# Kernel optimization log

Measured on AMD Instinct MI355X. Metric: run time of the kernel, lower is better.

Reference implementation:

```python
import jax, jax.numpy as jnp
import numpy as np

B, L, H, E = 4, 1024, 8, 64


def setup_inputs() -> dict:
    key = jax.random.key(0)
    kq, kk, kv = jax.random.split(key, 3)
    queries = jax.random.normal(kq, (B, L, H, E), dtype=jnp.float32)
    keys = jax.random.normal(kk, (B, L, H, E), dtype=jnp.float32)
    values = jax.random.normal(kv, (B, L, H, E), dtype=jnp.float32)
    attn_mask = jnp.zeros((1,), dtype=bool)  # unused by the module
    return {"queries": queries, "keys": keys, "values": values, "attn_mask": attn_mask}


def _spectral_interaction(queries, keys, values):
    # queries/keys/values: [B, L, H, E] (L == S here, so the torch truncation is a no-op)
    b, l, h, e = queries.shape
    qh = jnp.transpose(queries, (0, 2, 1, 3))  # [B,H,L,E]
    kh = jnp.transpose(keys[:, :l], (0, 2, 1, 3))  # [B,H,L,E]
    # cosine-similarity score matrix, exponentiated: exp(q.k / (|q||k|))
    q_norm = jnp.linalg.norm(qh, axis=-1, keepdims=True)  # [B,H,L,1]
    k_norm = jnp.linalg.norm(kh, axis=-1, keepdims=True)  # [B,H,L,1]
    dot_num = jnp.einsum('bhle,bhse->bhls', qh, kh)        # [B,H,L,L]
    dot_den = q_norm * jnp.swapaxes(k_norm, -1, -2)        # [B,H,L,L] via broadcast
    sim = jnp.exp(dot_num / dot_den)                       # [B,H,L,L]

    # FFT-domain double softmax over frequency bins
    inter_fft = jnp.fft.rfft(sim, axis=-1).real            # [B,H,L,F], F=L//2+1
    scale = 1.0 / np.sqrt(e)
    A = jax.nn.softmax(
        jnp.sum(jax.nn.softmax(scale * inter_fft, axis=-1), axis=-2),
        axis=-1,
    )                                                      # [B,H,F]  (dropout = identity in eval)
    A = A[:, :, None, :]                                   # [B,H,1,F]

    # gate the real part of the value spectrum, keep imag part, reconstruct
    vh = jnp.transpose(values[:, :l], (0, 2, 3, 1))        # [B,H,E,L]
    v_fft = jnp.fft.rfft(vh, axis=-1)                      # [B,H,E,F] complex
    Vc = jax.lax.complex(A * v_fft.real, v_fft.imag)       # [B,H,E,F]
    V = jnp.fft.irfft(Vc, n=l, axis=-1)                    # [B,H,E,L]
    return jnp.transpose(V, (0, 3, 2, 1))                  # [B,L,E,H] (matches torch permute(0,3,2,1))


def reference(queries, keys, values, attn_mask):
    # attn_mask is unused by the original forward
    return _spectral_interaction(queries, keys, values)
```

## Files before the change

### kernel.cpp

```cpp
#include <hip/hip_runtime.h>
#include <hip/hip_bf16.h>
#include <math.h>

#define B_ 4
#define L_ 1024
#define H_ 8
#define E_ 64
#define N_ 1024
#define NF_ 513
#define SCALE_ 0.125f
#define HE_ (H_ * E_)
#define ZP_ 1104

typedef _Float16 f16x8 __attribute__((ext_vector_type(8)));
typedef float f32x4 __attribute__((ext_vector_type(4)));

__device__ __forceinline__ int dr4(int x) {
    const int r = (int)(__brev((unsigned)x) >> 22);
    return ((r & 0x155) << 1) | ((r >> 1) & 0x155);
}

__device__ __forceinline__ int PD(int i) { return i + (i >> 4) + (i >> 6); }

__device__ __forceinline__ float2 cmulw(float2 v, float2 w, float dir) {
    const float wi = dir * w.y;
    return make_float2(v.x * w.x - v.y * wi, v.x * wi + v.y * w.x);
}

__device__ __forceinline__ void r4c(const float2 x0, const float2 x1,
                                    const float2 x2, const float2 x3,
                                    const float dir,
                                    float2& y0, float2& y1, float2& y2, float2& y3) {
    const float ax = x0.x + x2.x, ay = x0.y + x2.y;
    const float bx = x0.x - x2.x, by = x0.y - x2.y;
    const float cx = x1.x + x3.x, cy = x1.y + x3.y;
    const float dx = x1.x - x3.x, dy = x1.y - x3.y;
    y0 = make_float2(ax + cx, ay + cy);
    y2 = make_float2(ax - cx, ay - cy);
    y1 = make_float2(bx - dir * dy, by + dir * dx);
    y3 = make_float2(bx + dir * dy, by - dir * dx);
}

__device__ __forceinline__ void fill_tw(float2* tw, int t) {
    for (int i = t; i < 1024; i += 256) {
        float sv, cv;
        sincosf(6.283185307179586f * (float)i / 1024.0f, &sv, &cv);
        tw[PD(i)] = make_float2(cv, sv);
    }
}

__device__ __forceinline__ void wfft_dit4(float2* z, const float2* tw, int lane, float dir) {
    #pragma unroll
    for (int st = 0; st < 5; ++st) {
        const int l2q = 2 * st, qs = 1 << l2q;
        const int step = 1 << (8 - l2q);
        #pragma unroll
        for (int ib = 0; ib < 4; ++ib) {
            const int j = lane + 64 * ib;
            const int pos = j & (qs - 1);
            const int base = ((j >> l2q) << (l2q + 2)) + pos;
            const int i0 = PD(base), i1 = PD(base + qs), i2 = PD(base + 2 * qs), i3 = PD(base + 3 * qs);
            float2 x0 = z[i0], x1 = z[i1], x2 = z[i2], x3 = z[i3];
            if (st) {
                x1 = cmulw(x1, tw[PD(pos * step)], dir);
                x2 = cmulw(x2, tw[PD(2 * pos * step)], dir);
                x3 = cmulw(x3, tw[PD(3 * pos * step)], dir);
            }
            float2 y0, y1, y2, y3;
            r4c(x0, x1, x2, x3, dir, y0, y1, y2, y3);
            z[i0] = y0; z[i1] = y1; z[i2] = y2; z[i3] = y3;
        }
        __builtin_amdgcn_wave_barrier();
    }
}

__device__ __forceinline__ void wfft_dif4(float2* z, const float2* tw, int lane, float dir) {
    #pragma unroll
    for (int st = 4; st >= 0; --st) {
        const int l2q = 2 * st, qs = 1 << l2q;
        const int step = 1 << (8 - l2q);
        #pragma unroll
        for (int ib = 0; ib < 4; ++ib) {
            const int j = lane + 64 * ib;
            const int pos = j & (qs - 1);
            const int base = ((j >> l2q) << (l2q + 2)) + pos;
            const int i0 = PD(base), i1 = PD(base + qs), i2 = PD(base + 2 * qs), i3 = PD(base + 3 * qs);
            const float2 x0 = z[i0], x1 = z[i1], x2 = z[i2], x3 = z[i3];
            float2 s0, s1, s2, s3;
            r4c(x0, x1, x2, x3, dir, s0, s1, s2, s3);
            if (st) {
                s1 = cmulw(s1, tw[PD(pos * step)], dir);
                s2 = cmulw(s2, tw[PD(2 * pos * step)], dir);
                s3 = cmulw(s3, tw[PD(3 * pos * step)], dir);
            }
            z[i0] = s0; z[i1] = s1; z[i2] = s2; z[i3] = s3;
        }
        __builtin_amdgcn_wave_barrier();
    }
}

__global__ __launch_bounds__(256) void k_prep(const float* __restrict__ K,
                                              _Float16* __restrict__ Kh) {
    const int i = blockIdx.x * 256 + threadIdx.x;
    if (i >= B_ * L_ * H_) return;
    const float* p = K + (size_t)i * E_;
    float ss = 0.0f;
    #pragma unroll
    for (int j = 0; j < 16; ++j) {
        const float4 v = *(const float4*)(p + j * 4);
        ss += v.x * v.x + v.y * v.y + v.z * v.z + v.w * v.w;
    }
    const float r = rsqrtf(ss);
    _Float16* out = Kh + (size_t)i * E_;
    #pragma unroll
    for (int e = 0; e < E_; e += 8) {
        const float4 x = *(const float4*)(p + e);
        const float4 y = *(const float4*)(p + e + 4);
        f16x8 o;
        o[0] = (_Float16)(x.x * r); o[1] = (_Float16)(x.y * r);
        o[2] = (_Float16)(x.z * r); o[3] = (_Float16)(x.w * r);
        o[4] = (_Float16)(y.x * r); o[5] = (_Float16)(y.y * r);
        o[6] = (_Float16)(y.z * r); o[7] = (_Float16)(y.w * r);
        *(f16x8*)(out + e) = o;
    }
}

__global__ __attribute__((amdgpu_flat_work_group_size(256, 256), amdgpu_waves_per_eu(2, 3)))
void k_qkfft(const float* __restrict__ Q,
             const _Float16* __restrict__ Kh,
             float* __restrict__ G) {
    __shared__ float2 s_z[4 * ZP_];
    __shared__ float2 s_tw[ZP_];
    __shared__ float s_acc[NF_];

    const int t = threadIdx.x;
    const int bid = blockIdx.x;
    const int bh = bid >> 6;
    const int chunk = bid & 63;
    const int b = bh >> 3, h = bh & 7;
    const int l0 = chunk * 16;

    const int c = t & 15;
    const int g = (t >> 4) & 3;
    const int w = t >> 6;
    const int lane = t & 63;

    fill_tw(s_tw, t);
    for (int kk = t; kk < NF_; kk += 256) s_acc[kk] = 0.0f;

    const float* qrow = Q + (((size_t)b * L_ + l0 + c) * H_ + h) * E_;
    const float4 x0 = *(const float4*)(qrow + g * 8);
    const float4 y0 = *(const float4*)(qrow + g * 8 + 4);
    const float4 x1 = *(const float4*)(qrow + 32 + g * 8);
    const float4 y1 = *(const float4*)(qrow + 32 + g * 8 + 4);
    float ss = x0.x * x0.x + x0.y * x0.y + x0.z * x0.z + x0.w * x0.w
             + y0.x * y0.x + y0.y * y0.y + y0.z * y0.z + y0.w * y0.w
             + x1.x * x1.x + x1.y * x1.y + x1.z * x1.z + x1.w * x1.w
             + y1.x * y1.x + y1.y * y1.y + y1.z * y1.z + y1.w * y1.w;
    ss += __shfl_xor(ss, 16);
    ss += __shfl_xor(ss, 32);
    const float qn = rsqrtf(ss);
    f16x8 af0, af1;
    af0[0] = (_Float16)(x0.x * qn); af0[1] = (_Float16)(x0.y * qn);
    af0[2] = (_Float16)(x0.z * qn); af0[3] = (_Float16)(x0.w * qn);
    af0[4] = (_Float16)(y0.x * qn); af0[5] = (_Float16)(y0.y * qn);
    af0[6] = (_Float16)(y0.z * qn); af0[7] = (_Float16)(y0.w * qn);
    af1[0] = (_Float16)(x1.x * qn); af1[1] = (_Float16)(x1.y * qn);
    af1[2] = (_Float16)(x1.z * qn); af1[3] = (_Float16)(x1.w * qn);
    af1[4] = (_Float16)(y1.x * qn); af1[5] = (_Float16)(y1.y * qn);
    af1[6] = (_Float16)(y1.z * qn); af1[7] = (_Float16)(y1.w * qn);

    f32x4 acc[16];
    #pragma unroll
    for (int n = 0; n < 16; ++n) acc[n] = (f32x4){0.0f, 0.0f, 0.0f, 0.0f};

    #pragma unroll
    for (int n = 0; n < 16; ++n) {
        const int j = w * 256 + n * 16 + c;
        const int s = dr4(j);
        const f16x8* bp = (const f16x8*)(Kh + (((size_t)b * L_ + s) * H_ + h) * E_);
        const f16x8 b0 = bp[g];
        const f16x8 b1 = bp[4 + g];
        acc[n] = __builtin_amdgcn_mfma_f32_16x16x32_f16(af0, b0, acc[n], 0, 0, 0);
        acc[n] = __builtin_amdgcn_mfma_f32_16x16x32_f16(af1, b1, acc[n], 0, 0, 0);
        if ((n & 3) == 3) __builtin_amdgcn_sched_barrier(0);
    }

    #pragma unroll
    for (int n = 0; n < 16; ++n) {
        #pragma unroll
        for (int r = 0; r < 4; ++r) acc[n][r] = __expf(acc[n][r]);
    }

    float gacc[8];
    #pragma unroll
    for (int ib = 0; ib < 8; ++ib) gacc[ib] = 0.0f;
    float gN = 0.0f;

    float2* zw = s_z + w * ZP_;
    const float dir = -1.0f;

    #pragma unroll
    for (int rr = 0; rr < 2; ++rr) {
        __syncthreads();
        {
            const int gq = g - 2 * rr;
            if (gq == 0 || gq == 1) {
                float2* z01 = s_z + (2 * gq) * ZP_;
                #pragma unroll
                for (int n = 0; n < 16; ++n) {
                    const int ps = PD(w * 256 + n * 16 + c);
                    z01[ps]       = make_float2(acc[n][0], acc[n][1]);
                    z01[ZP_ + ps] = make_float2(acc[n][2], acc[n][3]);
                }
            }
        }
        __syncthreads();

        wfft_dit4(zw, s_tw, lane, dir);

        const float mA = SCALE_ * zw[0].x;
        const float mB = SCALE_ * zw[0].y;
        float pA[8], pB[8], sA = 0.0f, sB = 0.0f;
        #pragma unroll
        for (int ib = 0; ib < 8; ++ib) {
            const int k = lane + 64 * ib;
            const int kp = (N_ - k) & (N_ - 1);
            const float2 X1 = zw[PD(k)];
            const float2 X2 = zw[PD(kp)];
            pA[ib] = __expf(SCALE_ * 0.5f * (X1.x + X2.x) - mA);
            pB[ib] = __expf(SCALE_ * 0.5f * (X1.y + X2.y) - mB);
            sA += pA[ib]; sB += pB[ib];
        }
        float pAN = 0.0f, pBN = 0.0f;
        if (lane == 0) {
            const float2 XN = zw[PD(512)];
            pAN = __expf(SCALE_ * XN.x - mA);
            pBN = __expf(SCALE_ * XN.y - mB);
            sA += pAN; sB += pBN;
        }
        #pragma unroll
        for (int off = 32; off > 0; off >>= 1) {
            sA += __shfl_xor(sA, off);
            sB += __shfl_xor(sB, off);
        }
        const float iA = 1.0f / sA, iB = 1.0f / sB;
        #pragma unroll
        for (int ib = 0; ib < 8; ++ib) gacc[ib] += pA[ib] * iA + pB[ib] * iB;
        if (lane == 0) gN += pAN * iA + pBN * iB;
    }

    #pragma unroll
    for (int ib = 0; ib < 8; ++ib) atomicAdd(&s_acc[lane + 64 * ib], gacc[ib]);
    if (lane == 0) atomicAdd(&s_acc[512], gN);
    __syncthreads();

    float* Gp = G + (size_t)bh * NF_;
    for (int kk = t; kk < NF_; kk += 256) atomicAdd(&Gp[kk], s_acc[kk]);
}

__global__ __launch_bounds__(256) void k_vfft(const float* __restrict__ V,
                                              const float* __restrict__ G,
                                              float* __restrict__ Out) {
    __shared__ float2 s_zv[4 * ZP_];
    __shared__ float2 s_tw[ZP_];
    __shared__ float s_A[NF_];
    __shared__ float s_red[8];

    const int t = threadIdx.x;
    const int bid = blockIdx.x;
    const int bh = bid >> 3, pg = bid & 7;
    const int b = bh >> 3, h = bh & 7;
    const int w = t >> 6, lane = t & 63;
    const int e0 = 2 * (pg * 4 + w);

    fill_tw(s_tw, t);

    {
        const float* Gp = G + (size_t)bh * NF_;
        const float g0 = Gp[t];
        const float g1 = Gp[t + 256];
        const float g2 = (t == 0) ? Gp[512] : -1e30f;
        float m = fmaxf(fmaxf(g0, g1), g2);
        #pragma unroll
        for (int off = 32; off > 0; off >>= 1) m = fmaxf(m, __shfl_xor(m, off));
        if (lane == 0) s_red[w] = m;
        __syncthreads();
        m = fmaxf(fmaxf(s_red[0], s_red[1]), fmaxf(s_red[2], s_red[3]));
        const float p0 = __expf(g0 - m), p1 = __expf(g1 - m);
        const float p2 = (t == 0) ? __expf(g2 - m) : 0.0f;
        float s = p0 + p1 + p2;
        #pragma unroll
        for (int off = 32; off > 0; off >>= 1) s += __shfl_xor(s, off);
        __syncthreads();
        if (lane == 0) s_red[4 + w] = s;
        __syncthreads();
        s = s_red[4] + s_red[5] + s_red[6] + s_red[7];
        const float inv = 1.0f / s;
        s_A[t] = p0 * inv;
        s_A[t + 256] = p1 * inv;
        if (t == 0) s_A[512] = p2 * inv;
    }
    __syncthreads();

    float2* z = s_zv + w * ZP_;

    #pragma unroll
    for (int jb = 0; jb < 16; ++jb) {
        const int s = lane + 64 * jb;
        const float* vp = V + (((size_t)b * L_ + s) * H_ + h) * E_ + e0;
        z[PD(dr4(s))] = make_float2(vp[0], vp[1]);
    }
    __builtin_amdgcn_wave_barrier();

    wfft_dit4(z, s_tw, lane, -1.0f);

    #pragma unroll
    for (int ib = 0; ib < 8; ++ib) {
        const int k = lane + 64 * ib;
        const int kp = (N_ - k) & (N_ - 1);
        const int ik = PD(k), ikp = PD(kp);
        const float2 X1 = z[ik];
        const float2 X2 = z[ikp];
        const float reV1 = 0.5f * (X1.x + X2.x);
        const float imV1 = 0.5f * (X1.y - X2.y);
        const float reV2 = 0.5f * (X1.y + X2.y);
        const float imV2 = 0.5f * (X2.x - X1.x);
        const float a = s_A[k];
        z[ik] = make_float2(a * reV1 - imV2, imV1 + a * reV2);
        if (kp != k)
            z[ikp] = make_float2(a * reV1 + imV2, -imV1 + a * reV2);
    }
    if (lane == 0) {
        const float2 X = z[PD(512)];
        const float a = s_A[512];
        z[PD(512)] = make_float2(a * X.x, a * X.y);
    }
    __builtin_amdgcn_wave_barrier();

    wfft_dif4(z, s_tw, lane, +1.0f);

    const float invN = 1.0f / (float)N_;
    #pragma unroll
    for (int jb = 0; jb < 16; ++jb) {
        const int p = lane + 64 * jb;
        const int l = dr4(p);
        const float2 r = z[PD(p)];
        const size_t o = (((size_t)b * L_ + l) * E_ + e0) * H_ + h;
        Out[o] = r.x * invN;
        Out[o + H_] = r.y * invN;
    }
}

extern "C" void kernel_launch(void* const* d_in, const int* in_sizes, int n_in,
                              void* d_out, int out_size, void* d_ws, size_t ws_size,
                              hipStream_t stream) {
    const float* Q = (const float*)d_in[0];
    const float* K = (const float*)d_in[1];
    const float* V = (const float*)d_in[2];
    float* out = (float*)d_out;

    float* ws = (float*)d_ws;
    float* G     = ws;
    _Float16* Kh = (_Float16*)(ws + B_ * H_ * NF_);

    hipMemsetAsync(G, 0, (size_t)B_ * H_ * NF_ * sizeof(float), stream);
    k_prep<<<(B_ * L_ * H_ + 255) / 256, 256, 0, stream>>>(K, Kh);
    k_qkfft<<<B_ * H_ * (L_ / 16), 256, 0, stream>>>(Q, Kh, G);
    k_vfft<<<B_ * H_ * (E_ / 8), 256, 0, stream>>>(V, G, out);
}
```

Baseline: 136.4 us.

## Halve FFT shared buffer and run block-cooperative FFT over four rounds

The QK-FFT kernel stops having each of its four waves run its own 1024-point FFT on a private shared buffer. Instead the whole 256-thread block cooperates on two packed FFTs per round, with a barrier between radix-4 stages, over four serial rounds, and softmax sums are reduced across waves through a small shared array. This halves the s_z shared allocation and raises the waves-per-EU hint, aiming for more resident blocks per CU. The cost is many more __syncthreads per block and four serialized rounds instead of two.

```diff
diff --git a/kernel.cpp b/kernel.cpp
--- a/kernel.cpp
+++ b/kernel.cpp
@@ -125,13 +125,14 @@
     }
 }
 
-__global__ __attribute__((amdgpu_flat_work_group_size(256, 256), amdgpu_waves_per_eu(2, 3)))
+__global__ __attribute__((amdgpu_flat_work_group_size(256, 256), amdgpu_waves_per_eu(2, 5)))
 void k_qkfft(const float* __restrict__ Q,
              const _Float16* __restrict__ Kh,
              float* __restrict__ G) {
-    __shared__ float2 s_z[4 * ZP_];
+    __shared__ float2 s_z[2 * ZP_];
     __shared__ float2 s_tw[ZP_];
     __shared__ float s_acc[NF_];
+    __shared__ float s_red[16];
 
     const int t = threadIdx.x;
     const int bid = blockIdx.x;
@@ -143,7 +144,7 @@
     const int c = t & 15;
     const int g = (t >> 4) & 3;
     const int w = t >> 6;
-    const int lane = t & 63;
+    const int lane = t & 63, wid = w;
 
     fill_tw(s_tw, t);
     for (int kk = t; kk < NF_; kk += 256) s_acc[kk] = 0.0f;
@@ -192,67 +193,88 @@
         for (int r = 0; r < 4; ++r) acc[n][r] = __expf(acc[n][r]);
     }
 
-    float gacc[8];
-    #pragma unroll
-    for (int ib = 0; ib < 8; ++ib) gacc[ib] = 0.0f;
-    float gN = 0.0f;
-
-    float2* zw = s_z + w * ZP_;
     const float dir = -1.0f;
 
-    #pragma unroll
-    for (int rr = 0; rr < 2; ++rr) {
-        __syncthreads();
-        {
-            const int gq = g - 2 * rr;
-            if (gq == 0 || gq == 1) {
-                float2* z01 = s_z + (2 * gq) * ZP_;
-                #pragma unroll
-                for (int n = 0; n < 16; ++n) {
-                    const int ps = PD(w * 256 + n * 16 + c);
-                    z01[ps]       = make_float2(acc[n][0], acc[n][1]);
-                    z01[ZP_ + ps] = make_float2(acc[n][2], acc[n][3]);
-                }
-            }
-        }
-        __syncthreads();
-
-        wfft_dit4(zw, s_tw, lane, dir);
-
-        const float mA = SCALE_ * zw[0].x;
-        const float mB = SCALE_ * zw[0].y;
-        float pA[8], pB[8], sA = 0.0f, sB = 0.0f;
-        #pragma unroll
-        for (int ib = 0; ib < 8; ++ib) {
-            const int k = lane + 64 * ib;
-            const int kp = (N_ - k) & (N_ - 1);
-            const float2 X1 = zw[PD(k)];
-            const float2 X2 = zw[PD(kp)];
-            pA[ib] = __expf(SCALE_ * 0.5f * (X1.x + X2.x) - mA);
-            pB[ib] = __expf(SCALE_ * 0.5f * (X1.y + X2.y) - mB);
-            sA += pA[ib]; sB += pB[ib];
-        }
-        float pAN = 0.0f, pBN = 0.0f;
+    #pragma unroll 1
+    for (int rr = 0; rr < 4; ++rr) {
+        __syncthreads();
+        if (g == rr) {
+            #pragma unroll
+            for (int n = 0; n < 16; ++n) {
+                const int ps = PD(w * 256 + n * 16 + c);
+                s_z[ps]       = make_float2(acc[n][0], acc[n][1]);
+                s_z[ZP_ + ps] = make_float2(acc[n][2], acc[n][3]);
+            }
+        }
+        __syncthreads();
+
+        #pragma unroll
+        for (int st = 0; st < 5; ++st) {
+            const int l2q = 2 * st, qs = 1 << l2q;
+            const int pos = t & (qs - 1);
+            const int base = ((t >> l2q) << (l2q + 2)) + pos;
+            const int i0 = PD(base), i1 = PD(base + qs), i2 = PD(base + 2 * qs), i3 = PD(base + 3 * qs);
+            float2 w1, w2, w3;
+            if (st) {
+                const int step = 1 << (8 - l2q);
+                w1 = s_tw[PD(pos * step)];
+                w2 = s_tw[PD(2 * pos * step)];
+                w3 = s_tw[PD(3 * pos * step)];
+            }
+            #pragma unroll
+            for (int q = 0; q < 2; ++q) {
+                float2* z = s_z + q * ZP_;
+                float2 a0 = z[i0], a1 = z[i1], a2 = z[i2], a3 = z[i3];
+                if (st) { a1 = cmulw(a1, w1, dir); a2 = cmulw(a2, w2, dir); a3 = cmulw(a3, w3, dir); }
+                float2 b0, b1, b2, b3;
+                r4c(a0, a1, a2, a3, dir, b0, b1, b2, b3);
+                z[i0] = b0; z[i1] = b1; z[i2] = b2; z[i3] = b3;
+            }
+            __syncthreads();
+        }
+
+        const int iT = PD(t), iTn = PD((N_ - t) & (N_ - 1));
+        const int iU = PD(t + 256), iUn = PD(768 - t);
+        float p[4][2], pm[4], sm[4];
+        #pragma unroll
+        for (int q = 0; q < 2; ++q) {
+            const float2* z = s_z + q * ZP_;
+            const float2 X0 = z[iT], X0n = z[iTn], X1 = z[iU], X1n = z[iUn];
+            const float2 DC = z[0];
+            const float2 XN = z[PD(512)];
+            const float mA = SCALE_ * DC.x, mB = SCALE_ * DC.y;
+            p[2 * q][0]     = __expf(SCALE_ * 0.5f * (X0.x + X0n.x) - mA);
+            p[2 * q][1]     = __expf(SCALE_ * 0.5f * (X1.x + X1n.x) - mA);
+            p[2 * q + 1][0] = __expf(SCALE_ * 0.5f * (X0.y + X0n.y) - mB);
+            p[2 * q + 1][1] = __expf(SCALE_ * 0.5f * (X1.y + X1n.y) - mB);
+            pm[2 * q]     = __expf(SCALE_ * XN.x - mA);
+            pm[2 * q + 1] = __expf(SCALE_ * XN.y - mB);
+            sm[2 * q]     = p[2 * q][0] + p[2 * q][1] + ((t == 0) ? pm[2 * q] : 0.0f);
+            sm[2 * q + 1] = p[2 * q + 1][0] + p[2 * q + 1][1] + ((t == 0) ? pm[2 * q + 1] : 0.0f);
+        }
+        #pragma unroll
+        for (int off = 32; off > 0; off >>= 1) {
+            #pragma unroll
+            for (int q2 = 0; q2 < 4; ++q2) sm[q2] += __shfl_xor(sm[q2], off);
+        }
         if (lane == 0) {
-            const float2 XN = zw[PD(512)];
-            pAN = __expf(SCALE_ * XN.x - mA);
-            pBN = __expf(SCALE_ * XN.y - mB);
-            sA += pAN; sB += pBN;
-        }
-        #pragma unroll
-        for (int off = 32; off > 0; off >>= 1) {
-            sA += __shfl_xor(sA, off);
-            sB += __shfl_xor(sB, off);
-        }
-        const float iA = 1.0f / sA, iB = 1.0f / sB;
-        #pragma unroll
-        for (int ib = 0; ib < 8; ++ib) gacc[ib] += pA[ib] * iA + pB[ib] * iB;
-        if (lane == 0) gN += pAN * iA + pBN * iB;
-    }
-
-    #pragma unroll
-    for (int ib = 0; ib < 8; ++ib) atomicAdd(&s_acc[lane + 64 * ib], gacc[ib]);
-    if (lane == 0) atomicAdd(&s_acc[512], gN);
+            #pragma unroll
+            for (int q2 = 0; q2 < 4; ++q2) s_red[4 * q2 + wid] = sm[q2];
+        }
+        __syncthreads();
+        float add0 = 0.0f, add1 = 0.0f, addm = 0.0f;
+        #pragma unroll
+        for (int q2 = 0; q2 < 4; ++q2) {
+            const float inv = 1.0f / (s_red[4 * q2] + s_red[4 * q2 + 1] +
+                                      s_red[4 * q2 + 2] + s_red[4 * q2 + 3]);
+            add0 += p[q2][0] * inv;
+            add1 += p[q2][1] * inv;
+            addm += pm[q2] * inv;
+        }
+        s_acc[t]       += add0;
+        s_acc[t + 256] += add1;
+        if (t == 0) s_acc[512] += addm;
+    }
     __syncthreads();
 
     float* Gp = G + (size_t)bh * NF_;
```

After: 123.7 us. 1.1x faster.

## Replace per-row FFT of similarity rows with cosine-DFT matmul on MFMA

Applied to the files above, without the earlier changes.

The real part of the rFFT of each similarity row is now computed as a matmul against a precomputed fp16 cosine table on MFMA units, replacing the shared-memory radix-4 FFT. The similarity tile is staged in LDS as fp16, and the softmax max shift uses the DC bin, which is the row sum. Block size doubles to 32 query rows, and the per-bin reductions now go straight to global atomics. This adds a cosine-table kernel, reduces precision through fp16 cosines and fp16 exp values, and does roughly 4x more arithmetic than the FFT, relying on matrix-core throughput to cover it.

```diff
diff --git a/kernel.cpp b/kernel.cpp
--- a/kernel.cpp
+++ b/kernel.cpp
@@ -1,5 +1,6 @@
 #include <hip/hip_runtime.h>
 #include <hip/hip_bf16.h>
+#include <hip/hip_fp16.h>
 #include <math.h>
 
 #define B_ 4
@@ -11,22 +12,22 @@
 #define SCALE_ 0.125f
 #define HE_ (H_ * E_)
 #define ZP_ 1104
+#define NBPAD_ 576
+#define SIMP_ 1032
 
 typedef _Float16 f16x8 __attribute__((ext_vector_type(8)));
+typedef _Float16 f16x4 __attribute__((ext_vector_type(4)));
 typedef float f32x4 __attribute__((ext_vector_type(4)));
 
 __device__ __forceinline__ int dr4(int x) {
     const int r = (int)(__brev((unsigned)x) >> 22);
     return ((r & 0x155) << 1) | ((r >> 1) & 0x155);
 }
-
 __device__ __forceinline__ int PD(int i) { return i + (i >> 4) + (i >> 6); }
-
 __device__ __forceinline__ float2 cmulw(float2 v, float2 w, float dir) {
     const float wi = dir * w.y;
     return make_float2(v.x * w.x - v.y * wi, v.x * wi + v.y * w.x);
 }
-
 __device__ __forceinline__ void r4c(const float2 x0, const float2 x1,
                                     const float2 x2, const float2 x3,
                                     const float dir,
@@ -40,7 +41,6 @@
     y1 = make_float2(bx - dir * dy, by + dir * dx);
     y3 = make_float2(bx + dir * dy, by - dir * dx);
 }
-
 __device__ __forceinline__ void fill_tw(float2* tw, int t) {
     for (int i = t; i < 1024; i += 256) {
         float sv, cv;
@@ -48,7 +48,6 @@
         tw[PD(i)] = make_float2(cv, sv);
     }
 }
-
 __device__ __forceinline__ void wfft_dit4(float2* z, const float2* tw, int lane, float dir) {
     #pragma unroll
     for (int st = 0; st < 5; ++st) {
@@ -56,7 +55,8 @@
         const int step = 1 << (8 - l2q);
         #pragma unroll
         for (int ib = 0; ib < 4; ++ib) {
-            const int j = lane + 64 * ib;
+            const int j = (st == 0) ? (((lane & 15) << 2) | (lane >> 4)) + 64 * ib
+                                    : lane + 64 * ib;
             const int pos = j & (qs - 1);
             const int base = ((j >> l2q) << (l2q + 2)) + pos;
             const int i0 = PD(base), i1 = PD(base + qs), i2 = PD(base + 2 * qs), i3 = PD(base + 3 * qs);
@@ -73,7 +73,6 @@
         __builtin_amdgcn_wave_barrier();
     }
 }
-
 __device__ __forceinline__ void wfft_dif4(float2* z, const float2* tw, int lane, float dir) {
     #pragma unroll
     for (int st = 4; st >= 0; --st) {
@@ -81,7 +80,8 @@
         const int step = 1 << (8 - l2q);
         #pragma unroll
         for (int ib = 0; ib < 4; ++ib) {
-            const int j = lane + 64 * ib;
+            const int j = (st == 0) ? (((lane & 15) << 2) | (lane >> 4)) + 64 * ib
+                                    : lane + 64 * ib;
             const int pos = j & (qs - 1);
             const int base = ((j >> l2q) << (l2q + 2)) + pos;
             const int i0 = PD(base), i1 = PD(base + qs), i2 = PD(base + 2 * qs), i3 = PD(base + 3 * qs);
@@ -99,6 +99,23 @@
     }
 }
 
+__global__ __launch_bounds__(256) void k_ccos(_Float16* __restrict__ Cc) {
+    const int bin = blockIdx.x;
+    const int t = threadIdx.x;
+    f16x4 o;
+    if (bin > 512) {
+        o[0] = o[1] = o[2] = o[3] = (_Float16)0.0f;
+    } else {
+        #pragma unroll
+        for (int j = 0; j < 4; ++j) {
+            const int s = 4 * t + j;
+            const int m = (bin * s) & 1023;
+            o[j] = (_Float16)cosf((float)m * 0.006135923151542565f);
+        }
+    }
+    *(f16x4*)(Cc + (size_t)bin * 1024 + 4 * t) = o;
+}
+
 __global__ __launch_bounds__(256) void k_prep(const float* __restrict__ K,
                                               _Float16* __restrict__ Kh) {
     const int i = blockIdx.x * 256 + threadIdx.x;
@@ -125,138 +142,175 @@
     }
 }
 
-__global__ __attribute__((amdgpu_flat_work_group_size(256, 256), amdgpu_waves_per_eu(2, 3)))
+template<int NU>
+__device__ __forceinline__ void qk_group(const _Float16* __restrict__ Cc,
+                                         const _Float16* __restrict__ s_sim,
+                                         int ntb, int c, int g,
+                                         float F0a, float F0b,
+                                         float& rs0, float& rs1,
+                                         __half2 (&e)[NU * 4]) {
+    f32x4 acc[2][NU];
+    #pragma unroll
+    for (int u = 0; u < NU; ++u) {
+        acc[0][u] = (f32x4){0.f, 0.f, 0.f, 0.f};
+        acc[1][u] = (f32x4){0.f, 0.f, 0.f, 0.f};
+    }
+    #pragma unroll 4
+    for (int kt = 0; kt < 32; ++kt) {
+        const int ko = kt * 32 + g * 8;
+        const f16x8 B0 = *(const f16x8*)(s_sim + (size_t)c * SIMP_ + ko);
+        const f16x8 B1 = *(const f16x8*)(s_sim + (size_t)(16 + c) * SIMP_ + ko);
+        #pragma unroll
+        for (int u = 0; u < NU; ++u) {
+            const f16x8 A = *(const f16x8*)(Cc + (size_t)((ntb + u) * 16 + c) * 1024 + ko);
+            acc[0][u] = __builtin_amdgcn_mfma_f32_16x16x32_f16(A, B0, acc[0][u], 0, 0, 0);
+            acc[1][u] = __builtin_amdgcn_mfma_f32_16x16x32_f16(A, B1, acc[1][u], 0, 0, 0);
+        }
+    }
+    #pragma unroll
+    for (int u = 0; u < NU; ++u) {
+        #pragma unroll
+        for (int r = 0; r < 4; ++r) {
+            const int bin = (ntb + u) * 16 + 4 * g + r;
+            const float e0 = __expf(SCALE_ * (acc[0][u][r] - F0a));
+            const float e1 = __expf(SCALE_ * (acc[1][u][r] - F0b));
+            if (bin <= 512) { rs0 += e0; rs1 += e1; }
+            e[u * 4 + r] = __floats2half2_rn(e0, e1);
+        }
+    }
+}
+
+template<int NU>
+__device__ __forceinline__ void qk_accum(float* __restrict__ Gp,
+                                         const __half2 (&e)[NU * 4],
+                                         int ntb, int c, int g,
+                                         float inva, float invb) {
+    #pragma unroll
+    for (int u = 0; u < NU; ++u) {
+        #pragma unroll
+        for (int r = 0; r < 4; ++r) {
+            const int bin = (ntb + u) * 16 + 4 * g + r;
+            const float2 ef = __half22float2(e[u * 4 + r]);
+            float v = ef.x * inva + ef.y * invb;
+            v += __shfl_xor(v, 1);
+            v += __shfl_xor(v, 2);
+            v += __shfl_xor(v, 4);
+            v += __shfl_xor(v, 8);
+            if (c == 0 && bin <= 512) atomicAdd(&Gp[bin], v);
+        }
+    }
+}
+
+__global__ __attribute__((amdgpu_flat_work_group_size(256, 256), amdgpu_waves_per_eu(2, 2)))
 void k_qkfft(const float* __restrict__ Q,
              const _Float16* __restrict__ Kh,
+             const _Float16* __restrict__ Cc,
              float* __restrict__ G) {
-    __shared__ float2 s_z[4 * ZP_];
-    __shared__ float2 s_tw[ZP_];
-    __shared__ float s_acc[NF_];
+    __shared__ _Float16 s_sim[32 * SIMP_];
+    __shared__ float s_F0p[4][32];
+    __shared__ float s_F0[32];
+    __shared__ float s_rs[4][32];
+    __shared__ float s_inv[32];
 
     const int t = threadIdx.x;
     const int bid = blockIdx.x;
-    const int bh = bid >> 6;
-    const int chunk = bid & 63;
+    const int bh = bid >> 5;
+    const int l0 = (bid & 31) * 32;
     const int b = bh >> 3, h = bh & 7;
-    const int l0 = chunk * 16;
-
     const int c = t & 15;
     const int g = (t >> 4) & 3;
     const int w = t >> 6;
-    const int lane = t & 63;
-
-    fill_tw(s_tw, t);
-    for (int kk = t; kk < NF_; kk += 256) s_acc[kk] = 0.0f;
-
-    const float* qrow = Q + (((size_t)b * L_ + l0 + c) * H_ + h) * E_;
-    const float4 x0 = *(const float4*)(qrow + g * 8);
-    const float4 y0 = *(const float4*)(qrow + g * 8 + 4);
-    const float4 x1 = *(const float4*)(qrow + 32 + g * 8);
-    const float4 y1 = *(const float4*)(qrow + 32 + g * 8 + 4);
-    float ss = x0.x * x0.x + x0.y * x0.y + x0.z * x0.z + x0.w * x0.w
-             + y0.x * y0.x + y0.y * y0.y + y0.z * y0.z + y0.w * y0.w
-             + x1.x * x1.x + x1.y * x1.y + x1.z * x1.z + x1.w * x1.w
-             + y1.x * y1.x + y1.y * y1.y + y1.z * y1.z + y1.w * y1.w;
-    ss += __shfl_xor(ss, 16);
-    ss += __shfl_xor(ss, 32);
-    const float qn = rsqrtf(ss);
-    f16x8 af0, af1;
-    af0[0] = (_Float16)(x0.x * qn); af0[1] = (_Float16)(x0.y * qn);
-    af0[2] = (_Float16)(x0.z * qn); af0[3] = (_Float16)(x0.w * qn);
-    af0[4] = (_Float16)(y0.x * qn); af0[5] = (_Float16)(y0.y * qn);
-    af0[6] = (_Float16)(y0.z * qn); af0[7] = (_Float16)(y0.w * qn);
-    af1[0] = (_Float16)(x1.x * qn); af1[1] = (_Float16)(x1.y * qn);
-    af1[2] = (_Float16)(x1.z * qn); af1[3] = (_Float16)(x1.w * qn);
-    af1[4] = (_Float16)(y1.x * qn); af1[5] = (_Float16)(y1.y * qn);
-    af1[6] = (_Float16)(y1.z * qn); af1[7] = (_Float16)(y1.w * qn);
-
-    f32x4 acc[16];
-    #pragma unroll
-    for (int n = 0; n < 16; ++n) acc[n] = (f32x4){0.0f, 0.0f, 0.0f, 0.0f};
-
-    #pragma unroll
-    for (int n = 0; n < 16; ++n) {
-        const int j = w * 256 + n * 16 + c;
-        const int s = dr4(j);
-        const f16x8* bp = (const f16x8*)(Kh + (((size_t)b * L_ + s) * H_ + h) * E_);
-        const f16x8 b0 = bp[g];
-        const f16x8 b1 = bp[4 + g];
-        acc[n] = __builtin_amdgcn_mfma_f32_16x16x32_f16(af0, b0, acc[n], 0, 0, 0);
-        acc[n] = __builtin_amdgcn_mfma_f32_16x16x32_f16(af1, b1, acc[n], 0, 0, 0);
-        if ((n & 3) == 3) __builtin_amdgcn_sched_barrier(0);
-    }
-
-    #pragma unroll
-    for (int n = 0; n < 16; ++n) {
-        #pragma unroll
-        for (int r = 0; r < 4; ++r) acc[n][r] = __expf(acc[n][r]);
-    }
-
-    float gacc[8];
-    #pragma unroll
-    for (int ib = 0; ib < 8; ++ib) gacc[ib] = 0.0f;
-    float gN = 0.0f;
-
-    float2* zw = s_z + w * ZP_;
-    const float dir = -1.0f;
-
-    #pragma unroll
-    for (int rr = 0; rr < 2; ++rr) {
-        __syncthreads();
-        {
-            const int gq = g - 2 * rr;
-            if (gq == 0 || gq == 1) {
-                float2* z01 = s_z + (2 * gq) * ZP_;
-                #pragma unroll
-                for (int n = 0; n < 16; ++n) {
-                    const int ps = PD(w * 256 + n * 16 + c);
-                    z01[ps]       = make_float2(acc[n][0], acc[n][1]);
-                    z01[ZP_ + ps] = make_float2(acc[n][2], acc[n][3]);
-                }
+
+    float p0[2][4];
+    #pragma unroll
+    for (int m = 0; m < 2; ++m)
+        #pragma unroll
+        for (int r = 0; r < 4; ++r) p0[m][r] = 0.0f;
+
+    #pragma unroll
+    for (int m = 0; m < 2; ++m) {
+        const float* qrow = Q + (((size_t)b * L_ + l0 + 16 * m + c) * H_ + h) * E_;
+        const float4 x0 = *(const float4*)(qrow + g * 8);
+        const float4 y0 = *(const float4*)(qrow + g * 8 + 4);
+        const float4 x1 = *(const float4*)(qrow + 32 + g * 8);
+        const float4 y1 = *(const float4*)(qrow + 32 + g * 8 + 4);
+        float ss = x0.x * x0.x + x0.y * x0.y + x0.z * x0.z + x0.w * x0.w
+                 + y0.x * y0.x + y0.y * y0.y + y0.z * y0.z + y0.w * y0.w
+                 + x1.x * x1.x + x1.y * x1.y + x1.z * x1.z + x1.w * x1.w
+                 + y1.x * y1.x + y1.y * y1.y + y1.z * y1.z + y1.w * y1.w;
+        ss += __shfl_xor(ss, 16);
+        ss += __shfl_xor(ss, 32);
+        const float qn = rsqrtf(ss);
+        f16x8 af0, af1;
+        af0[0] = (_Float16)(x0.x * qn); af0[1] = (_Float16)(x0.y * qn);
+        af0[2] = (_Float16)(x0.z * qn); af0[3] = (_Float16)(x0.w * qn);
+        af0[4] = (_Float16)(y0.x * qn); af0[5] = (_Float16)(y0.y * qn);
+        af0[6] = (_Float16)(y0.z * qn); af0[7] = (_Float16)(y0.w * qn);
+        af1[0] = (_Float16)(x1.x * qn); af1[1] = (_Float16)(x1.y * qn);
+        af1[2] = (_Float16)(x1.z * qn); af1[3] = (_Float16)(x1.w * qn);
+        af1[4] = (_Float16)(y1.x * qn); af1[5] = (_Float16)(y1.y * qn);
+        af1[6] = (_Float16)(y1.z * qn); af1[7] = (_Float16)(y1.w * qn);
+
+        #pragma unroll
+        for (int i = 0; i < 16; ++i) {
+            const int nt = w * 16 + i;
+            const f16x8* bp = (const f16x8*)(Kh + (((size_t)b * L_ + nt * 16 + c) * H_ + h) * E_);
+            f32x4 acc = (f32x4){0.f, 0.f, 0.f, 0.f};
+            acc = __builtin_amdgcn_mfma_f32_16x16x32_f16(af0, bp[g], acc, 0, 0, 0);
+            acc = __builtin_amdgcn_mfma_f32_16x16x32_f16(af1, bp[4 + g], acc, 0, 0, 0);
+            #pragma unroll
+            for (int r = 0; r < 4; ++r) {
+                const float ev = __expf(acc[r]);
+                p0[m][r] += ev;
+                s_sim[(size_t)(16 * m + 4 * g + r) * SIMP_ + nt * 16 + c] = (_Float16)ev;
             }
         }
-        __syncthreads();
-
-        wfft_dit4(zw, s_tw, lane, dir);
-
-        const float mA = SCALE_ * zw[0].x;
-        const float mB = SCALE_ * zw[0].y;
-        float pA[8], pB[8], sA = 0.0f, sB = 0.0f;
-        #pragma unroll
-        for (int ib = 0; ib < 8; ++ib) {
-            const int k = lane + 64 * ib;
-            const int kp = (N_ - k) & (N_ - 1);
-            const float2 X1 = zw[PD(k)];
-            const float2 X2 = zw[PD(kp)];
-            pA[ib] = __expf(SCALE_ * 0.5f * (X1.x + X2.x) - mA);
-            pB[ib] = __expf(SCALE_ * 0.5f * (X1.y + X2.y) - mB);
-            sA += pA[ib]; sB += pB[ib];
-        }
-        float pAN = 0.0f, pBN = 0.0f;
-        if (lane == 0) {
-            const float2 XN = zw[PD(512)];
-            pAN = __expf(SCALE_ * XN.x - mA);
-            pBN = __expf(SCALE_ * XN.y - mB);
-            sA += pAN; sB += pBN;
-        }
-        #pragma unroll
-        for (int off = 32; off > 0; off >>= 1) {
-            sA += __shfl_xor(sA, off);
-            sB += __shfl_xor(sB, off);
-        }
-        const float iA = 1.0f / sA, iB = 1.0f / sB;
-        #pragma unroll
-        for (int ib = 0; ib < 8; ++ib) gacc[ib] += pA[ib] * iA + pB[ib] * iB;
-        if (lane == 0) gN += pAN * iA + pBN * iB;
-    }
-
-    #pragma unroll
-    for (int ib = 0; ib < 8; ++ib) atomicAdd(&s_acc[lane + 64 * ib], gacc[ib]);
-    if (lane == 0) atomicAdd(&s_acc[512], gN);
+    }
+    #pragma unroll
+    for (int m = 0; m < 2; ++m)
+        #pragma unroll
+        for (int r = 0; r < 4; ++r) {
+            float v = p0[m][r];
+            v += __shfl_xor(v, 1);
+            v += __shfl_xor(v, 2);
+            v += __shfl_xor(v, 4);
+            v += __shfl_xor(v, 8);
+            p0[m][r] = v;
+        }
+    if (c == 0) {
+        #pragma unroll
+        for (int m = 0; m < 2; ++m)
+            #pragma unroll
+            for (int r = 0; r < 4; ++r)
+                s_F0p[w][16 * m + 4 * g + r] = p0[m][r];
+    }
     __syncthreads();
+    if (t < 32) s_F0[t] = s_F0p[0][t] + s_F0p[1][t] + s_F0p[2][t] + s_F0p[3][t];
+    __syncthreads();
+
+    const float F0a = s_F0[c];
+    const float F0b = s_F0[16 + c];
+
+    float rs0 = 0.0f, rs1 = 0.0f;
+    __half2 eG0[16], eG1[16], eS[4];
+    const int nt0 = w * 9;
+    qk_group<4>(Cc, s_sim, nt0,     c, g, F0a, F0b, rs0, rs1, eG0);
+    qk_group<4>(Cc, s_sim, nt0 + 4, c, g, F0a, F0b, rs0, rs1, eG1);
+    qk_group<1>(Cc, s_sim, nt0 + 8, c, g, F0a, F0b, rs0, rs1, eS);
+
+    rs0 += __shfl_xor(rs0, 16); rs0 += __shfl_xor(rs0, 32);
+    rs1 += __shfl_xor(rs1, 16); rs1 += __shfl_xor(rs1, 32);
+    if (g == 0) { s_rs[w][c] = rs0; s_rs[w][16 + c] = rs1; }
+    __syncthreads();
+    if (t < 32) s_inv[t] = 1.0f / (s_rs[0][t] + s_rs[1][t] + s_rs[2][t] + s_rs[3][t]);
+    __syncthreads();
+    const float inva = s_inv[c];
+    const float invb = s_inv[16 + c];
 
     float* Gp = G + (size_t)bh * NF_;
-    for (int kk = t; kk < NF_; kk += 256) atomicAdd(&Gp[kk], s_acc[kk]);
+    qk_accum<4>(Gp, eG0, nt0,     c, g, inva, invb);
+    qk_accum<4>(Gp, eG1, nt0 + 4, c, g, inva, invb);
+    qk_accum<1>(Gp, eS,  nt0 + 8, c, g, inva, invb);
 }
 
 __global__ __launch_bounds__(256) void k_vfft(const float* __restrict__ V,
@@ -361,11 +415,13 @@
     float* out = (float*)d_out;
 
     float* ws = (float*)d_ws;
-    float* G     = ws;
-    _Float16* Kh = (_Float16*)(ws + B_ * H_ * NF_);
+    float* G      = ws;
+    _Float16* Kh  = (_Float16*)(ws + B_ * H_ * NF_);
+    _Float16* Cc  = Kh + (size_t)B_ * L_ * H_ * E_;
 
     hipMemsetAsync(G, 0, (size_t)B_ * H_ * NF_ * sizeof(float), stream);
+    k_ccos<<<NBPAD_, 256, 0, stream>>>(Cc);
     k_prep<<<(B_ * L_ * H_ + 255) / 256, 256, 0, stream>>>(K, Kh);
-    k_qkfft<<<B_ * H_ * (L_ / 16), 256, 0, stream>>>(Q, Kh, G);
+    k_qkfft<<<B_ * H_ * (L_ / 32), 256, 0, stream>>>(Q, Kh, Cc, G);
     k_vfft<<<B_ * H_ * (E_ / 8), 256, 0, stream>>>(V, G, out);
 }
```

After: 224.1 us. 64.3% more time.
